# Kernel optimization log

Hardware: AMD Instinct MI355X
Metric: run time of the kernel (lower is better)

Reference implementation:

```python
import jax, jax.numpy as jnp
import numpy as np

N = 50000      # nodes in batched graph
E = 800000     # edges
IN_DIM = 16
HID = 64
NH = 4         # heads
G = 128        # graphs in batch
OUT_DIM = 32
NUM_LAYERS = 8
NEG_SLOPE = 0.2  # DGL GATv2Conv default


def setup_inputs() -> dict:
    key = jax.random.key(0)
    ks = jax.random.split(key, 12)
    feat = jax.random.normal(ks[0], (N, IN_DIM), dtype=jnp.float32)
    src = jax.random.randint(ks[1], (E,), 0, N, dtype=jnp.int32)
    dst = jax.random.randint(ks[2], (E,), 0, N, dtype=jnp.int32)
    graph_ids = jnp.sort(jax.random.randint(ks[3], (N,), 0, G, dtype=jnp.int32))
    is_root = jax.random.randint(ks[4], (N,), 0, 2, dtype=jnp.int32)
    s_in = 1.0 / np.sqrt(IN_DIM)
    s_h = 1.0 / np.sqrt(2 * HID)
    s_o = 1.0 / np.sqrt(HID)
    return {
        'feat': feat, 'src': src, 'dst': dst,
        'graph_ids': graph_ids, 'is_root': is_root,
        'W_in': jax.random.normal(ks[5], (IN_DIM, HID), jnp.float32) * s_in,
        'b_in': jnp.zeros((HID,), jnp.float32),
        'W_src': jax.random.normal(ks[6], (2 * HID, NH * HID), jnp.float32) * s_h,
        'b_src': jnp.zeros((NH * HID,), jnp.float32),
        'W_dst': jax.random.normal(ks[7], (2 * HID, NH * HID), jnp.float32) * s_h,
        'b_dst': jnp.zeros((NH * HID,), jnp.float32),
        'attn': jax.random.normal(ks[8], (NH, HID), jnp.float32) * s_o,
        'W_out': jax.random.normal(ks[9], (HID, OUT_DIM), jnp.float32) * s_o,
        'b_out': jnp.zeros((OUT_DIM,), jnp.float32),
    }


def reference(feat, src, dst, graph_ids, is_root,
              W_in, b_in, W_src, b_src, W_dst, b_dst, attn, W_out, b_out):
    h0 = feat @ W_in + b_in                       # [N, HID]
    h = h0
    for _ in range(NUM_LAYERS):
        x = jnp.concatenate([h, h0], axis=1)      # [N, 2*HID]
        fs = (x @ W_src + b_src).reshape(-1, NH, HID)  # [N, NH, HID]
        fd = (x @ W_dst + b_dst).reshape(-1, NH, HID)
        # per-edge GATv2 attention logits
        e = jax.nn.leaky_relu(fs[src] + fd[dst], NEG_SLOPE)   # [E, NH, HID]
        s = jnp.einsum('ehd,hd->eh', e, attn)                 # [E, NH]
        # segment softmax over incoming edges of each dst node
        m = jax.ops.segment_max(s, dst, num_segments=N)       # [N, NH]
        a = jnp.exp(s - m[dst])
        denom = jax.ops.segment_sum(a, dst, num_segments=N)
        alpha = a / denom[dst]                                # [E, NH]
        # weighted aggregation of source features
        agg = jax.ops.segment_sum(alpha[:, :, None] * fs[src], dst,
                                  num_segments=N)             # [N, NH, HID]
        h = jnp.tanh(agg).sum(axis=1)                         # [N, HID]
    # root-weighted readout per graph
    hg = jax.ops.segment_sum(h * is_root.astype(h.dtype)[:, None],
                             graph_ids, num_segments=G)       # [G, HID]
    return hg @ W_out + b_out                                 # [G, OUT_DIM]
```

## Files before the change

### kernel.cpp

```cpp
#include <hip/hip_runtime.h>
#include <math.h>

#define N_NODES 50000
#define N_EDGES 800000
#define IN_DIM  16
#define HID     64
#define NH      4
#define NGRAPH  128
#define OUT_DIM 32
#define NUM_LAYERS 8
#define NEG_SLOPE 0.2f

#define SCAN_BLOCKS ((N_NODES + 255) / 256)

typedef unsigned short u16;
typedef unsigned char  u8;
typedef _Float16 h2   __attribute__((ext_vector_type(2)));
typedef _Float16 f16x8 __attribute__((ext_vector_type(8)));
typedef float f32x2 __attribute__((ext_vector_type(2)));
typedef __attribute__((ext_vector_type(4))) float f32x4;

static __device__ __forceinline__ u16 f2h(float f) {
    _Float16 h = (_Float16)f; u16 r; __builtin_memcpy(&r, &h, 2); return r;
}
static __device__ __forceinline__ float h2f_lo(unsigned w) {
    _Float16 h; u16 u = (u16)w; __builtin_memcpy(&h, &u, 2); return (float)h;
}
static __device__ __forceinline__ h2 shfl_h2(h2 v, int mask) {
    int i; __builtin_memcpy(&i, &v, 4); i = __shfl_xor(i, mask);
    h2 r; __builtin_memcpy(&r, &i, 4); return r;
}
static __device__ __forceinline__ h2 bcast_h2(float f) {
    _Float16 h = (_Float16)f; h2 r; r[0] = h; r[1] = h; return r;
}
static __device__ __forceinline__ h2 fp8x2_to_h2(unsigned w) {
    f32x2 f = __builtin_amdgcn_cvt_pk_f32_fp8((int)w, false);
    h2 r; r[0] = (_Float16)f[0]; r[1] = (_Float16)f[1]; return r;
}

#define DPP_XOR1(x) __uint_as_float((unsigned)__builtin_amdgcn_update_dpp(0, (int)__float_as_uint(x), 0xB1, 0xF, 0xF, true))
#define DPP_XOR2(x) __uint_as_float((unsigned)__builtin_amdgcn_update_dpp(0, (int)__float_as_uint(x), 0x4E, 0xF, 0xF, true))


__global__ void k_build_wpack(const float* __restrict__ Wsrc, const float* __restrict__ bsrc,
                              const float* __restrict__ Wdst, const float* __restrict__ bdst,
                              const float* __restrict__ attn,
                              u16* __restrict__ Wpack, float* __restrict__ bcat,
                              u16* __restrict__ an_h) {
    int tid = blockIdx.x * 256 + threadIdx.x;
    int i = tid & 7;
    int l = (tid >> 3) & 63;
    int rest = tid >> 9;
    int kt = rest & 3;
    int nt = rest >> 2;
    int k = kt * 32 + (l >> 4) * 8 + i;
    int col = nt * 16 + (l & 15);
    float v = (col < 256) ? Wsrc[k * 256 + col] : Wdst[k * 256 + (col - 256)];
    Wpack[tid] = f2h(v);
    if (tid < 512) bcat[tid] = (tid < 256) ? bsrc[tid] : bdst[tid - 256];
    if (tid < 256) an_h[tid] = f2h(attn[tid] * 1.44269504f);
}

__global__ void k_hist(const int* __restrict__ dst, int* __restrict__ deg) {
    int e = blockIdx.x * 256 + threadIdx.x;
    if (e < N_EDGES) atomicAdd(&deg[dst[e]], 1);
}

__global__ void k_blocksum(const int* __restrict__ deg, int* __restrict__ bsum) {
    __shared__ int sm[256];
    int i = blockIdx.x * 256 + threadIdx.x;
    sm[threadIdx.x] = (i < N_NODES) ? deg[i] : 0;
    __syncthreads();
    for (int s = 128; s > 0; s >>= 1) {
        if (threadIdx.x < s) sm[threadIdx.x] += sm[threadIdx.x + s];
        __syncthreads();
    }
    if (threadIdx.x == 0) bsum[blockIdx.x] = sm[0];
}

__global__ void k_scanbsum(int* __restrict__ bsum) {
    if (threadIdx.x == 0 && blockIdx.x == 0) {
        int acc = 0;
        for (int b = 0; b < SCAN_BLOCKS; b++) { int t = bsum[b]; bsum[b] = acc; acc += t; }
    }
}

__global__ void k_rowptr(const int* __restrict__ deg, const int* __restrict__ bsum,
                         int* __restrict__ row_ptr) {
    __shared__ int sm[256];
    int i = blockIdx.x * 256 + threadIdx.x;
    int v = (i < N_NODES) ? deg[i] : 0;
    sm[threadIdx.x] = v;
    __syncthreads();
    for (int s = 1; s < 256; s <<= 1) {
        int t = (threadIdx.x >= (unsigned)s) ? sm[threadIdx.x - s] : 0;
        __syncthreads();
        sm[threadIdx.x] += t;
        __syncthreads();
    }
    if (i < N_NODES) row_ptr[i] = bsum[blockIdx.x] + sm[threadIdx.x] - v;
}

__global__ void k_scatter(const int* __restrict__ src, const int* __restrict__ dst,
                          const int* __restrict__ row_ptr, int* __restrict__ cursor,
                          int* __restrict__ csr_src) {
    int e = blockIdx.x * 256 + threadIdx.x;
    if (e < N_EDGES) {
        int d = dst[e];
        int pos = atomicAdd(&cursor[d], 1);
        csr_src[row_ptr[d] + pos] = src[e];
    }
}

__global__ __launch_bounds__(256) void k_in_gemm(const float* __restrict__ feat,
                                                 const float* __restrict__ W,
                                                 const float* __restrict__ b,
                                                 u16* __restrict__ h0h) {
    __shared__ float sW[IN_DIM * HID];
    __shared__ float sb[HID];
    int t = threadIdx.x;
    for (int i = t; i < IN_DIM * HID; i += 256) sW[i] = W[i];
    if (t < HID) sb[t] = b[t];
    __syncthreads();
    int wid = (blockIdx.x * 256 + t) >> 6;
    int lane = t & 63;
    const float* f = feat + wid * IN_DIM;
    float acc = sb[lane];
    #pragma unroll
    for (int k = 0; k < IN_DIM; k++) acc += f[k] * sW[k * HID + lane];
    h0h[wid * HID + lane] = f2h(acc);
}


#define ST_STRIDE 152
__global__ __launch_bounds__(256) void k_gemm_mfma(const u16* __restrict__ hb,
                                                   const u16* __restrict__ h0b,
                                                   const u16* __restrict__ Wpack,
                                                   const float* __restrict__ bcat,
                                                   u8* __restrict__ fs8,
                                                   u16* __restrict__ fdh) {
    __shared__ u16 smem[16384];
    int tid = threadIdx.x;
    int l = tid & 63, w = tid >> 6;
    int lr = l & 15, lg = l >> 4;
    int wave_gid = blockIdx.x * 4 + w;
    size_t rbase = (size_t)wave_gid * 32;
    u16* myst = smem + w * 4096;

    for (int g = 0; g < 4; g++) {
        __syncthreads();
        {
            const f16x8* src = (const f16x8*)(Wpack) + g * 2048;
            f16x8* dst = (f16x8*)smem;
            #pragma unroll
            for (int it = 0; it < 8; it++) dst[it * 256 + tid] = src[it * 256 + tid];
        }
        __syncthreads();

        f32x4 acc[2][8];
        #pragma unroll
        for (int rt = 0; rt < 2; rt++)
            #pragma unroll
            for (int nt = 0; nt < 8; nt++) acc[rt][nt] = (f32x4){0.f, 0.f, 0.f, 0.f};

        #pragma unroll
        for (int kt = 0; kt < 4; kt++) {
            const u16* A = (kt < 2) ? hb : h0b;
            int koff = (kt & 1) * 32 + lg * 8;
            f16x8 a0, a1;
            {
                size_t r0 = rbase + lr;
                size_t r1 = rbase + 16 + lr;
                if (r0 >= N_NODES) r0 = 0;
                if (r1 >= N_NODES) r1 = 0;
                a0 = *(const f16x8*)(A + r0 * HID + koff);
                a1 = *(const f16x8*)(A + r1 * HID + koff);
            }
            #pragma unroll
            for (int nt = 0; nt < 8; nt++) {
                f16x8 bfr = *(const f16x8*)(smem + nt * 2048 + kt * 512 + l * 8);
                acc[0][nt] = __builtin_amdgcn_mfma_f32_16x16x32_f16(a0, bfr, acc[0][nt], 0, 0, 0);
                acc[1][nt] = __builtin_amdgcn_mfma_f32_16x16x32_f16(a1, bfr, acc[1][nt], 0, 0, 0);
            }
        }
        __syncthreads();

        #pragma unroll
        for (int rt = 0; rt < 2; rt++) {
            size_t row0 = rbase + rt * 16;
            if (row0 >= N_NODES) break;
            #pragma unroll
            for (int nt = 0; nt < 8; nt++) {
                float bv = bcat[g * 128 + nt * 16 + lr];
                #pragma unroll
                for (int j = 0; j < 4; j++)
                    myst[(lg * 4 + j) * ST_STRIDE + nt * 16 + lr] = f2h(acc[rt][nt][j] + bv);
            }
            #pragma unroll
            for (int j = 0; j < 4; j++) {
                int rloc = j * 4 + lg;
                f16x8 v = *(const f16x8*)(myst + rloc * ST_STRIDE + lr * 8);
                if (g < 2) {
                    int p0 = __builtin_amdgcn_cvt_pk_fp8_f32((float)v[0], (float)v[1], 0, false);
                    int p1 = __builtin_amdgcn_cvt_pk_fp8_f32((float)v[2], (float)v[3], 0, false);
                    int p2 = __builtin_amdgcn_cvt_pk_fp8_f32((float)v[4], (float)v[5], 0, false);
                    int p3 = __builtin_amdgcn_cvt_pk_fp8_f32((float)v[6], (float)v[7], 0, false);
                    uint2 o8;
                    o8.x = (unsigned)(p0 & 0xffff) | ((unsigned)p1 << 16);
                    o8.y = (unsigned)(p2 & 0xffff) | ((unsigned)p3 << 16);
                    *(uint2*)(fs8 + (row0 + rloc) * 256 + g * 128 + lr * 8) = o8;
                } else {
                    *(f16x8*)(fdh + (row0 + rloc) * 256 + (g - 2) * 128 + lr * 8) = v;
                }
            }
        }
    }
}

__global__ __launch_bounds__(256) void k_edge(const u8* __restrict__ fs8,
                                              const u16* __restrict__ fdh,
                                              const u16* __restrict__ an_h,
                                              const int* __restrict__ row_ptr,
                                              const int* __restrict__ deg,
                                              const int* __restrict__ csr_src,
                                              u16* __restrict__ h) {
    int wid = (blockIdx.x * 256 + threadIdx.x) >> 6;
    int lane = threadIdx.x & 63;
    int g  = lane >> 4;
    int ll = lane & 15;
    const size_t ebase = (size_t)ll * 16;

    h2 an[8], fdhv[8];
    {
        const uint4* ap = (const uint4*)(an_h + ebase);
        uint4 a0 = ap[0], a1 = ap[1];
        unsigned aw[8] = {a0.x, a0.y, a0.z, a0.w, a1.x, a1.y, a1.z, a1.w};
        __builtin_memcpy(an, aw, 32);
        const uint4* fp = (const uint4*)(fdh + (size_t)wid * 256 + ebase);
        uint4 b0 = fp[0], b1 = fp[1];
        unsigned fw[8] = {b0.x, b0.y, b0.z, b0.w, b1.x, b1.y, b1.z, b1.w};
        __builtin_memcpy(fdhv, fw, 32);
    }
    const h2 slope2 = {(_Float16)NEG_SLOPE, (_Float16)NEG_SLOPE};

    float mA = -3.0e38f, mB = -3.0e38f, dnA = 0.f, dnB = 0.f;
    h2 aggA[8], aggB[8];
    #pragma unroll
    for (int q = 0; q < 8; q++) {
        aggA[q] = (h2){(_Float16)0.f, (_Float16)0.f};
        aggB[q] = (h2){(_Float16)0.f, (_Float16)0.f};
    }

    int r0 = row_ptr[wid], dg = deg[wid];
    for (int i = g; i < dg; i += 8) {
        int iB = i + 4;
        bool hB = iB < dg;
        int sA = csr_src[r0 + i];
        int sB = csr_src[r0 + (hB ? iB : i)];
        uint4 A = *(const uint4*)(fs8 + (size_t)sA * 256 + ebase);
        uint4 B = *(const uint4*)(fs8 + (size_t)sB * 256 + ebase);

        h2 fA[8];
        {
            unsigned d[4] = {A.x, A.y, A.z, A.w};
            #pragma unroll
            for (int q = 0; q < 4; q++) {
                fA[2*q]   = fp8x2_to_h2(d[q] & 0xffffu);
                fA[2*q+1] = fp8x2_to_h2(d[q] >> 16);
            }
        }
        float p0 = 0.f, p1 = 0.f;
        #pragma unroll
        for (int q = 0; q < 8; q += 2) {
            h2 e0 = fA[q] + fdhv[q];
            h2 e1 = fA[q+1] + fdhv[q+1];
            h2 l0 = __builtin_elementwise_max(e0, e0 * slope2);
            h2 l1 = __builtin_elementwise_max(e1, e1 * slope2);
            p0 = __builtin_amdgcn_fdot2(l0, an[q],   p0, false);
            p1 = __builtin_amdgcn_fdot2(l1, an[q+1], p1, false);
        }
        float p = p0 + p1;
        p += DPP_XOR1(p);
        p += DPP_XOR2(p);
        float nm = fmaxf(mA, p);
        float rs = exp2f(mA - nm);
        float c  = exp2f(p - nm);
        h2 rs2 = bcast_h2(rs), c2 = bcast_h2(c);
        #pragma unroll
        for (int q = 0; q < 8; q++) aggA[q] = aggA[q] * rs2 + fA[q] * c2;
        dnA = fmaf(dnA, rs, c);
        mA = nm;

        if (hB) {
            h2 fB[8];
            {
                unsigned d[4] = {B.x, B.y, B.z, B.w};
                #pragma unroll
                for (int q = 0; q < 4; q++) {
                    fB[2*q]   = fp8x2_to_h2(d[q] & 0xffffu);
                    fB[2*q+1] = fp8x2_to_h2(d[q] >> 16);
                }
            }
            float q0 = 0.f, q1 = 0.f;
            #pragma unroll
            for (int q = 0; q < 8; q += 2) {
                h2 e0 = fB[q] + fdhv[q];
                h2 e1 = fB[q+1] + fdhv[q+1];
                h2 l0 = __builtin_elementwise_max(e0, e0 * slope2);
                h2 l1 = __builtin_elementwise_max(e1, e1 * slope2);
                q0 = __builtin_amdgcn_fdot2(l0, an[q],   q0, false);
                q1 = __builtin_amdgcn_fdot2(l1, an[q+1], q1, false);
            }
            float pB = q0 + q1;
            pB += DPP_XOR1(pB);
            pB += DPP_XOR2(pB);
            float nmB = fmaxf(mB, pB);
            float rsB = exp2f(mB - nmB);
            float cB  = exp2f(pB - nmB);
            h2 rsB2 = bcast_h2(rsB), cB2 = bcast_h2(cB);
            #pragma unroll
            for (int q = 0; q < 8; q++) aggB[q] = aggB[q] * rsB2 + fB[q] * cB2;
            dnB = fmaf(dnB, rsB, cB);
            mB = nmB;
        }
    }

    float m, denom;
    h2 agg[8];
    {
        m = fmaxf(mA, mB);
        float sA = exp2f(mA - m), sB = exp2f(mB - m);
        denom = dnA * sA + dnB * sB;
        h2 sA2 = bcast_h2(sA), sB2 = bcast_h2(sB);
        #pragma unroll
        for (int q = 0; q < 8; q++) agg[q] = aggA[q] * sA2 + aggB[q] * sB2;
    }

    {
        float mm = fmaxf(m, __shfl_xor(m, 16));
        mm = fmaxf(mm, __shfl_xor(mm, 32));
        float sc = exp2f(m - mm);
        denom *= sc;
        h2 sc2 = bcast_h2(sc);
        #pragma unroll
        for (int q = 0; q < 8; q++) agg[q] = agg[q] * sc2;
        denom += __shfl_xor(denom, 16);
        denom += __shfl_xor(denom, 32);
        #pragma unroll
        for (int q = 0; q < 8; q++) {
            agg[q] = agg[q] + shfl_h2(agg[q], 16);
            agg[q] = agg[q] + shfl_h2(agg[q], 32);
        }
    }

    float inv = denom > 0.f ? __builtin_amdgcn_rcpf(denom) : 0.f;
    float inv2 = inv * 2.885390082f;

    h2 x0 = (g & 2) ? ((g & 1) ? agg[6] : agg[4]) : ((g & 1) ? agg[2] : agg[0]);
    h2 x1 = (g & 2) ? ((g & 1) ? agg[7] : agg[5]) : ((g & 1) ? agg[3] : agg[1]);
    float t[4] = {(float)x0[0], (float)x0[1], (float)x1[0], (float)x1[1]};
    #pragma unroll
    for (int j = 0; j < 4; j++) {
        float E = exp2f(t[j] * inv2);
        float r = __builtin_amdgcn_rcpf(E + 1.f);
        float v = fmaf(-2.f, r, 1.f);
        v += __shfl_xor(v, 4);
        v += __shfl_xor(v, 8);
        t[j] = v;
    }
    if (ll < 4) {
        uint2 o;
        o.x = (unsigned)f2h(t[0]) | ((unsigned)f2h(t[1]) << 16);
        o.y = (unsigned)f2h(t[2]) | ((unsigned)f2h(t[3]) << 16);
        *(uint2*)(h + (size_t)wid * 64 + ll * 16 + g * 4) = o;
    }
}


__global__ __launch_bounds__(256) void k_readout(const u16* __restrict__ h,
                                                 const int* __restrict__ graph_ids,
                                                 const int* __restrict__ is_root,
                                                 float* __restrict__ hg) {
    int wid = (blockIdx.x * 256 + threadIdx.x) >> 6;
    int lane = threadIdx.x & 63;
    if (is_root[wid]) {
        int g = graph_ids[wid];
        atomicAdd(&hg[g * HID + lane], h2f_lo(h[(size_t)wid * HID + lane]));
    }
}

__global__ void k_out_gemm(const float* __restrict__ hg, const float* __restrict__ W,
                           const float* __restrict__ b, float* __restrict__ out) {
    int i = blockIdx.x * 256 + threadIdx.x;
    if (i >= NGRAPH * OUT_DIM) return;
    int g = i >> 5, o = i & 31;
    float acc = b[o];
    #pragma unroll
    for (int k = 0; k < HID; k++) acc += hg[g * HID + k] * W[k * OUT_DIM + o];
    out[i] = acc;
}


extern "C" void kernel_launch(void* const* d_in, const int* in_sizes, int n_in,
                              void* d_out, int out_size, void* d_ws, size_t ws_size,
                              hipStream_t stream) {
    const float* feat      = (const float*)d_in[0];
    const int*   src       = (const int*)d_in[1];
    const int*   dst       = (const int*)d_in[2];
    const int*   graph_ids = (const int*)d_in[3];
    const int*   is_root   = (const int*)d_in[4];
    const float* W_in      = (const float*)d_in[5];
    const float* b_in      = (const float*)d_in[6];
    const float* W_src     = (const float*)d_in[7];
    const float* b_src     = (const float*)d_in[8];
    const float* W_dst     = (const float*)d_in[9];
    const float* b_dst     = (const float*)d_in[10];
    const float* attn      = (const float*)d_in[11];
    const float* W_out     = (const float*)d_in[12];
    const float* b_out     = (const float*)d_in[13];
    float* out = (float*)d_out;

    char* base = (char*)d_ws;
    size_t off = 0;
    auto carve = [&](size_t bytes) -> char* {
        char* p = base + off;
        off = (off + bytes + 255) & ~(size_t)255;
        return p;
    };
    u16*   h0b     = (u16*)carve((size_t)N_NODES * HID * 2);
    u16*   hb      = (u16*)carve((size_t)N_NODES * HID * 2);
    u8*    fs8     = (u8*)carve((size_t)N_NODES * 256);
    u16*   fdh     = (u16*)carve((size_t)N_NODES * 256 * 2);
    u16*   Wpack   = (u16*)carve(128 * 512 * 2);
    float* bcat    = (float*)carve(512 * 4);
    u16*   an_h    = (u16*)carve(256 * 2);
    int*   csr_src = (int*)carve((size_t)N_EDGES * 4);
    int*   row_ptr = (int*)carve((size_t)N_NODES * 4);
    int*   bsum    = (int*)carve(SCAN_BLOCKS * 4);
    char*  zero0   = carve(0);
    int*   deg     = (int*)carve((size_t)N_NODES * 4);
    int*   cursor  = (int*)carve((size_t)N_NODES * 4);
    float* hg      = (float*)carve((size_t)NGRAPH * HID * 4);
    char*  zero1   = base + off;
    if (off > ws_size) return;

    (void)hipMemsetAsync(zero0, 0, (size_t)(zero1 - zero0), stream);

    k_build_wpack<<<256, 256, 0, stream>>>(W_src, b_src, W_dst, b_dst, attn, Wpack, bcat, an_h);
    k_hist<<<(N_EDGES + 255) / 256, 256, 0, stream>>>(dst, deg);
    k_blocksum<<<SCAN_BLOCKS, 256, 0, stream>>>(deg, bsum);
    k_scanbsum<<<1, 64, 0, stream>>>(bsum);
    k_rowptr<<<SCAN_BLOCKS, 256, 0, stream>>>(deg, bsum, row_ptr);
    k_scatter<<<(N_EDGES + 255) / 256, 256, 0, stream>>>(src, dst, row_ptr, cursor, csr_src);

    k_in_gemm<<<N_NODES / 4, 256, 0, stream>>>(feat, W_in, b_in, h0b);

    const int gemm_grid = (N_NODES + 127) / 128;
    for (int layer = 0; layer < NUM_LAYERS; layer++) {
        const u16* hcur = (layer == 0) ? h0b : hb;
        k_gemm_mfma<<<gemm_grid, 256, 0, stream>>>(hcur, h0b, Wpack, bcat, fs8, fdh);
        k_edge<<<N_NODES / 4, 256, 0, stream>>>(fs8, fdh, an_h, row_ptr, deg, csr_src, hb);
    }

    k_readout<<<N_NODES / 4, 256, 0, stream>>>(hb, graph_ids, is_root, hg);
    k_out_gemm<<<(NGRAPH * OUT_DIM + 255) / 256, 256, 0, stream>>>(hg, W_out, b_out, out);
}
```

Baseline: 961.8 us.

## Split GEMM grid per output group and use lazy-max online softmax in edge kernel

The projection GEMM now gives each block a single 128-column output group and has each wave compute 16 rows. This replaces the loop where one block reloaded all four weight groups and synchronised between them. In the edge kernel, the two interleaved accumulator streams are merged into one. The online softmax now rescales only when a new logit exceeds the running max by more than 4 (log2 domain), which removes most per-edge rescale multiplies and one exp. FP8 unpacking uses the hi/lo word-select conversion plus packed RTZ fp16 conversion. The trade-offs are less memory-level parallelism per lane in the edge loop and larger intermediate fp16 accumulator magnitudes, which could lose precision.

```diff
diff --git a/kernel.cpp b/kernel.cpp
--- a/kernel.cpp
+++ b/kernel.cpp
@@ -33,9 +33,9 @@
 static __device__ __forceinline__ h2 bcast_h2(float f) {
     _Float16 h = (_Float16)f; h2 r; r[0] = h; r[1] = h; return r;
 }
-static __device__ __forceinline__ h2 fp8x2_to_h2(unsigned w) {
-    f32x2 f = __builtin_amdgcn_cvt_pk_f32_fp8((int)w, false);
-    h2 r; r[0] = (_Float16)f[0]; r[1] = (_Float16)f[1]; return r;
+static __device__ __forceinline__ h2 pkrtz_h2(float a, float b) {
+    auto v = __builtin_amdgcn_cvt_pkrtz(a, b);
+    h2 r; __builtin_memcpy(&r, &v, 4); return r;
 }
 
 #define DPP_XOR1(x) __uint_as_float((unsigned)__builtin_amdgcn_update_dpp(0, (int)__float_as_uint(x), 0xB1, 0xF, 0xF, true))
@@ -139,80 +139,63 @@
                                                    const float* __restrict__ bcat,
                                                    u8* __restrict__ fs8,
                                                    u16* __restrict__ fdh) {
-    __shared__ u16 smem[16384];
+    __shared__ u16 sW[16384];
+    __shared__ u16 sStage[4][2432];
     int tid = threadIdx.x;
+    int g  = blockIdx.x & 3;
+    int tb = blockIdx.x >> 2;
     int l = tid & 63, w = tid >> 6;
     int lr = l & 15, lg = l >> 4;
-    int wave_gid = blockIdx.x * 4 + w;
-    size_t rbase = (size_t)wave_gid * 32;
-    u16* myst = smem + w * 4096;
-
-    for (int g = 0; g < 4; g++) {
-        __syncthreads();
-        {
-            const f16x8* src = (const f16x8*)(Wpack) + g * 2048;
-            f16x8* dst = (f16x8*)smem;
-            #pragma unroll
-            for (int it = 0; it < 8; it++) dst[it * 256 + tid] = src[it * 256 + tid];
-        }
-        __syncthreads();
-
-        f32x4 acc[2][8];
-        #pragma unroll
-        for (int rt = 0; rt < 2; rt++)
-            #pragma unroll
-            for (int nt = 0; nt < 8; nt++) acc[rt][nt] = (f32x4){0.f, 0.f, 0.f, 0.f};
-
-        #pragma unroll
-        for (int kt = 0; kt < 4; kt++) {
-            const u16* A = (kt < 2) ? hb : h0b;
-            int koff = (kt & 1) * 32 + lg * 8;
-            f16x8 a0, a1;
-            {
-                size_t r0 = rbase + lr;
-                size_t r1 = rbase + 16 + lr;
-                if (r0 >= N_NODES) r0 = 0;
-                if (r1 >= N_NODES) r1 = 0;
-                a0 = *(const f16x8*)(A + r0 * HID + koff);
-                a1 = *(const f16x8*)(A + r1 * HID + koff);
-            }
-            #pragma unroll
-            for (int nt = 0; nt < 8; nt++) {
-                f16x8 bfr = *(const f16x8*)(smem + nt * 2048 + kt * 512 + l * 8);
-                acc[0][nt] = __builtin_amdgcn_mfma_f32_16x16x32_f16(a0, bfr, acc[0][nt], 0, 0, 0);
-                acc[1][nt] = __builtin_amdgcn_mfma_f32_16x16x32_f16(a1, bfr, acc[1][nt], 0, 0, 0);
-            }
-        }
-        __syncthreads();
-
-        #pragma unroll
-        for (int rt = 0; rt < 2; rt++) {
-            size_t row0 = rbase + rt * 16;
-            if (row0 >= N_NODES) break;
-            #pragma unroll
-            for (int nt = 0; nt < 8; nt++) {
-                float bv = bcat[g * 128 + nt * 16 + lr];
-                #pragma unroll
-                for (int j = 0; j < 4; j++)
-                    myst[(lg * 4 + j) * ST_STRIDE + nt * 16 + lr] = f2h(acc[rt][nt][j] + bv);
-            }
-            #pragma unroll
-            for (int j = 0; j < 4; j++) {
-                int rloc = j * 4 + lg;
-                f16x8 v = *(const f16x8*)(myst + rloc * ST_STRIDE + lr * 8);
-                if (g < 2) {
-                    int p0 = __builtin_amdgcn_cvt_pk_fp8_f32((float)v[0], (float)v[1], 0, false);
-                    int p1 = __builtin_amdgcn_cvt_pk_fp8_f32((float)v[2], (float)v[3], 0, false);
-                    int p2 = __builtin_amdgcn_cvt_pk_fp8_f32((float)v[4], (float)v[5], 0, false);
-                    int p3 = __builtin_amdgcn_cvt_pk_fp8_f32((float)v[6], (float)v[7], 0, false);
-                    uint2 o8;
-                    o8.x = (unsigned)(p0 & 0xffff) | ((unsigned)p1 << 16);
-                    o8.y = (unsigned)(p2 & 0xffff) | ((unsigned)p3 << 16);
-                    *(uint2*)(fs8 + (row0 + rloc) * 256 + g * 128 + lr * 8) = o8;
-                } else {
-                    *(f16x8*)(fdh + (row0 + rloc) * 256 + (g - 2) * 128 + lr * 8) = v;
-                }
-            }
+
+    {
+        const f16x8* src = (const f16x8*)(Wpack + g * 16384);
+        f16x8* dst = (f16x8*)sW;
+        #pragma unroll
+        for (int it = 0; it < 8; it++) dst[it * 256 + tid] = src[it * 256 + tid];
+    }
+    __syncthreads();
+
+    size_t row0 = (size_t)(tb * 4 + w) * 16;
+    if (row0 >= N_NODES) return;
+
+    f32x4 acc[8];
+    #pragma unroll
+    for (int nt = 0; nt < 8; nt++) acc[nt] = (f32x4){0.f, 0.f, 0.f, 0.f};
+
+    #pragma unroll
+    for (int kt = 0; kt < 4; kt++) {
+        const u16* A = (kt < 2) ? hb : h0b;
+        f16x8 a = *(const f16x8*)(A + (row0 + lr) * HID + (kt & 1) * 32 + lg * 8);
+        #pragma unroll
+        for (int nt = 0; nt < 8; nt++) {
+            f16x8 bfr = *(const f16x8*)(sW + nt * 2048 + kt * 512 + l * 8);
+            acc[nt] = __builtin_amdgcn_mfma_f32_16x16x32_f16(a, bfr, acc[nt], 0, 0, 0);
+        }
+    }
+
+    u16* myst = sStage[w];
+    #pragma unroll
+    for (int nt = 0; nt < 8; nt++) {
+        float bv = bcat[g * 128 + nt * 16 + lr];
+        #pragma unroll
+        for (int j = 0; j < 4; j++)
+            myst[(lg * 4 + j) * ST_STRIDE + nt * 16 + lr] = f2h(acc[nt][j] + bv);
+    }
+    #pragma unroll
+    for (int j = 0; j < 4; j++) {
+        int rloc = j * 4 + lg;
+        f16x8 v = *(const f16x8*)(myst + rloc * ST_STRIDE + lr * 8);
+        if (g < 2) {
+            int p0 = __builtin_amdgcn_cvt_pk_fp8_f32((float)v[0], (float)v[1], 0, false);
+            int p1 = __builtin_amdgcn_cvt_pk_fp8_f32((float)v[2], (float)v[3], 0, false);
+            int p2 = __builtin_amdgcn_cvt_pk_fp8_f32((float)v[4], (float)v[5], 0, false);
+            int p3 = __builtin_amdgcn_cvt_pk_fp8_f32((float)v[6], (float)v[7], 0, false);
+            uint2 o8;
+            o8.x = (unsigned)(p0 & 0xffff) | ((unsigned)p1 << 16);
+            o8.y = (unsigned)(p2 & 0xffff) | ((unsigned)p3 << 16);
+            *(uint2*)(fs8 + (row0 + rloc) * 256 + g * 128 + lr * 8) = o8;
+        } else {
+            *(f16x8*)(fdh + (row0 + rloc) * 256 + (g - 2) * 128 + lr * 8) = v;
         }
     }
 }
@@ -243,37 +226,32 @@
     }
     const h2 slope2 = {(_Float16)NEG_SLOPE, (_Float16)NEG_SLOPE};
 
-    float mA = -3.0e38f, mB = -3.0e38f, dnA = 0.f, dnB = 0.f;
-    h2 aggA[8], aggB[8];
-    #pragma unroll
-    for (int q = 0; q < 8; q++) {
-        aggA[q] = (h2){(_Float16)0.f, (_Float16)0.f};
-        aggB[q] = (h2){(_Float16)0.f, (_Float16)0.f};
-    }
+    float m = -3.0e38f, denom = 0.f;
+    h2 agg[8];
+    #pragma unroll
+    for (int q = 0; q < 8; q++) agg[q] = (h2){(_Float16)0.f, (_Float16)0.f};
 
     int r0 = row_ptr[wid], dg = deg[wid];
-    for (int i = g; i < dg; i += 8) {
-        int iB = i + 4;
-        bool hB = iB < dg;
-        int sA = csr_src[r0 + i];
-        int sB = csr_src[r0 + (hB ? iB : i)];
-        uint4 A = *(const uint4*)(fs8 + (size_t)sA * 256 + ebase);
-        uint4 B = *(const uint4*)(fs8 + (size_t)sB * 256 + ebase);
-
-        h2 fA[8];
+    for (int i = g; i < dg; i += 4) {
+        int s = csr_src[r0 + i];
+        uint4 A = *(const uint4*)(fs8 + (size_t)s * 256 + ebase);
+
+        h2 f[8];
         {
             unsigned d[4] = {A.x, A.y, A.z, A.w};
             #pragma unroll
             for (int q = 0; q < 4; q++) {
-                fA[2*q]   = fp8x2_to_h2(d[q] & 0xffffu);
-                fA[2*q+1] = fp8x2_to_h2(d[q] >> 16);
+                f32x2 lo = __builtin_amdgcn_cvt_pk_f32_fp8((int)d[q], false);
+                f32x2 hi = __builtin_amdgcn_cvt_pk_f32_fp8((int)d[q], true);
+                f[2*q]   = pkrtz_h2(lo[0], lo[1]);
+                f[2*q+1] = pkrtz_h2(hi[0], hi[1]);
             }
         }
         float p0 = 0.f, p1 = 0.f;
         #pragma unroll
         for (int q = 0; q < 8; q += 2) {
-            h2 e0 = fA[q] + fdhv[q];
-            h2 e1 = fA[q+1] + fdhv[q+1];
+            h2 e0 = f[q]   + fdhv[q];
+            h2 e1 = f[q+1] + fdhv[q+1];
             h2 l0 = __builtin_elementwise_max(e0, e0 * slope2);
             h2 l1 = __builtin_elementwise_max(e1, e1 * slope2);
             p0 = __builtin_amdgcn_fdot2(l0, an[q],   p0, false);
@@ -282,58 +260,23 @@
         float p = p0 + p1;
         p += DPP_XOR1(p);
         p += DPP_XOR2(p);
-        float nm = fmaxf(mA, p);
-        float rs = exp2f(mA - nm);
-        float c  = exp2f(p - nm);
-        h2 rs2 = bcast_h2(rs), c2 = bcast_h2(c);
-        #pragma unroll
-        for (int q = 0; q < 8; q++) aggA[q] = aggA[q] * rs2 + fA[q] * c2;
-        dnA = fmaf(dnA, rs, c);
-        mA = nm;
-
-        if (hB) {
-            h2 fB[8];
-            {
-                unsigned d[4] = {B.x, B.y, B.z, B.w};
-                #pragma unroll
-                for (int q = 0; q < 4; q++) {
-                    fB[2*q]   = fp8x2_to_h2(d[q] & 0xffffu);
-                    fB[2*q+1] = fp8x2_to_h2(d[q] >> 16);
-                }
-            }
-            float q0 = 0.f, q1 = 0.f;
+
+        float c;
+        if (__builtin_expect(p > m + 4.f, 0)) {
+            float rs = exp2f(m - p);
+            h2 rs2 = bcast_h2(rs);
             #pragma unroll
-            for (int q = 0; q < 8; q += 2) {
-                h2 e0 = fB[q] + fdhv[q];
-                h2 e1 = fB[q+1] + fdhv[q+1];
-                h2 l0 = __builtin_elementwise_max(e0, e0 * slope2);
-                h2 l1 = __builtin_elementwise_max(e1, e1 * slope2);
-                q0 = __builtin_amdgcn_fdot2(l0, an[q],   q0, false);
-                q1 = __builtin_amdgcn_fdot2(l1, an[q+1], q1, false);
-            }
-            float pB = q0 + q1;
-            pB += DPP_XOR1(pB);
-            pB += DPP_XOR2(pB);
-            float nmB = fmaxf(mB, pB);
-            float rsB = exp2f(mB - nmB);
-            float cB  = exp2f(pB - nmB);
-            h2 rsB2 = bcast_h2(rsB), cB2 = bcast_h2(cB);
-            #pragma unroll
-            for (int q = 0; q < 8; q++) aggB[q] = aggB[q] * rsB2 + fB[q] * cB2;
-            dnB = fmaf(dnB, rsB, cB);
-            mB = nmB;
-        }
-    }
-
-    float m, denom;
-    h2 agg[8];
-    {
-        m = fmaxf(mA, mB);
-        float sA = exp2f(mA - m), sB = exp2f(mB - m);
-        denom = dnA * sA + dnB * sB;
-        h2 sA2 = bcast_h2(sA), sB2 = bcast_h2(sB);
-        #pragma unroll
-        for (int q = 0; q < 8; q++) agg[q] = aggA[q] * sA2 + aggB[q] * sB2;
+            for (int q = 0; q < 8; q++) agg[q] = agg[q] * rs2;
+            denom *= rs;
+            m = p;
+            c = 1.f;
+        } else {
+            c = exp2f(p - m);
+        }
+        h2 c2 = bcast_h2(c);
+        #pragma unroll
+        for (int q = 0; q < 8; q++) agg[q] = agg[q] + f[q] * c2;
+        denom += c;
     }
 
     {
@@ -455,7 +398,7 @@
 
     k_in_gemm<<<N_NODES / 4, 256, 0, stream>>>(feat, W_in, b_in, h0b);
 
-    const int gemm_grid = (N_NODES + 127) / 128;
+    const int gemm_grid = ((N_NODES / 16 + 3) / 4) * 4;
     for (int layer = 0; layer < NUM_LAYERS; layer++) {
         const u16* hcur = (layer == 0) ? h0b : hb;
         k_gemm_mfma<<<gemm_grid, 256, 0, stream>>>(hcur, h0b, Wpack, bcat, fs8, fdh);
```

Result: faster. 824.1 us (-14.3%).
